# Optimization experiments

Hardware: AMD Instinct MI355X
Metric: run time of the kernel (lower is better)

Reference implementation:

```python
import jax, jax.numpy as jnp
import numpy as np

B, S, D = 1, 2048, 1024
H, HD = 16, 64          # attention heads, head dim
DFF = 4096              # ffn hidden
IH, ID = 4, 64          # indexer heads / dim ('baseline' strategy)
TOP_K = 64
ROPE_BASE = 10000.0
LN_EPS = 1e-5


def setup_inputs() -> dict:
    key = jax.random.key(0)
    ks = jax.random.split(key, 12)
    g = lambda k, shape: (jax.random.normal(k, shape, dtype=jnp.float32) * 0.02)
    return {
        "x": jax.random.normal(ks[0], (B, S, D), dtype=jnp.float32),
        "w_qkv": g(ks[1], (D, 3 * D)),
        "w_o": g(ks[2], (D, D)),
        "ffn_w1": g(ks[3], (D, DFF)),
        "ffn_b1": jnp.zeros((DFF,), jnp.float32),
        "ffn_w2": g(ks[4], (DFF, D)),
        "ffn_b2": jnp.zeros((D,), jnp.float32),
        "ln1_g": jnp.ones((D,), jnp.float32),
        "ln1_b": jnp.zeros((D,), jnp.float32),
        "ln2_g": jnp.ones((D,), jnp.float32),
        "ln2_b": jnp.zeros((D,), jnp.float32),
        "idx_wq": g(ks[5], (D, IH * ID)),
        "idx_wk": g(ks[6], (D, ID)),
        "idx_ww": g(ks[7], (D, IH)),
    }


def _layernorm(x, g, b):
    m = jnp.mean(x, axis=-1, keepdims=True)
    v = jnp.var(x, axis=-1, keepdims=True)
    return (x - m) * jax.lax.rsqrt(v + LN_EPS) * g + b


def _rope(x):  # x: [B,S,H,HD], torchtune interleaved-pair convention
    half = HD // 2
    theta = 1.0 / (ROPE_BASE ** (jnp.arange(0, HD, 2, dtype=jnp.float32) / HD))  # [half]
    ang = jnp.arange(S, dtype=jnp.float32)[:, None] * theta                      # [S,half]
    cos = jnp.cos(ang)[None, :, None, :]
    sin = jnp.sin(ang)[None, :, None, :]
    xp = x.reshape(*x.shape[:-1], half, 2)
    x0, x1 = xp[..., 0], xp[..., 1]
    out = jnp.stack([x0 * cos - x1 * sin, x1 * cos + x0 * sin], axis=-1)
    return out.reshape(x.shape)


def reference(x, w_qkv, w_o, ffn_w1, ffn_b1, ffn_w2, ffn_b2,
              ln1_g, ln1_b, ln2_g, ln2_b, idx_wq, idx_wk, idx_ww):
    norm_x = _layernorm(x, ln1_g, ln1_b)

    qkv = norm_x @ w_qkv                              # [B,S,3D]
    q, k, v = jnp.split(qkv, 3, axis=-1)
    q = _rope(q.reshape(B, S, H, HD))
    k = _rope(k.reshape(B, S, H, HD))
    v = v.reshape(B, S, H, HD)

    # Lightning-style indexer: I[t,s] = sum_h w[t,h] * relu(q_i[t,h] . k_i[s])
    qi = (norm_x @ idx_wq).reshape(B, S, IH, ID)      # [B,S,IH,ID]
    ki = norm_x @ idx_wk                              # [B,S,ID]
    wi = norm_x @ idx_ww                              # [B,S,IH]
    qk = jnp.einsum("bthd,bsd->bths", qi, ki)         # [B,S,IH,S]
    index_scores = jnp.einsum("bth,bths->bts", wi, jax.nn.relu(qk))  # [B,S,S]

    # causal top-k token selection -> boolean mask
    causal = jnp.tril(jnp.ones((S, S), dtype=bool))
    masked_scores = jnp.where(causal, index_scores, -jnp.inf)
    _, topk_idx = jax.lax.top_k(masked_scores, TOP_K)  # [B,S,K]
    b_ix = jnp.arange(B)[:, None, None]
    q_ix = jnp.arange(S)[None, :, None]
    mask = jnp.zeros((B, S, S), dtype=bool).at[b_ix, q_ix, topk_idx].set(True)
    mask = mask & causal                               # [B,S,S]

    # masked SDPA
    logits = jnp.einsum("bqhd,bkhd->bhqk", q, k) / np.sqrt(HD)
    logits = jnp.where(mask[:, None, :, :], logits, -jnp.inf)
    attn = jax.nn.softmax(logits, axis=-1)
    attn_out = jnp.einsum("bhqk,bkhd->bqhd", attn, v).reshape(B, S, D)
    x = x + attn_out @ w_o

    h = _layernorm(x, ln2_g, ln2_b)
    ffn = jax.nn.gelu(h @ ffn_w1 + ffn_b1, approximate=False) @ ffn_w2 + ffn_b2
    return x + ffn
```

## Files before the change

kernel.cpp:

```cpp
#include <hip/hip_runtime.h>
#include <math.h>

#define S_LEN 2048
#define D_MODEL 1024
#define NHEAD 16
#define HDIM 64
#define DFF 4096
#define IH 4
#define IDM 64
#define TOPK 64
#define NIDX 336

typedef float f32x4 __attribute__((ext_vector_type(4)));
typedef short bf16x8 __attribute__((ext_vector_type(8)));

__device__ __forceinline__ unsigned short f2bf(float f) {
    unsigned u = __builtin_bit_cast(unsigned, f);
    u += 0x7fff + ((u >> 16) & 1);
    return (unsigned short)(u >> 16);
}
__device__ __forceinline__ float bf2f(unsigned short us) {
    return __builtin_bit_cast(float, (unsigned)us << 16);
}

__device__ __forceinline__ float gelu_exact(float v) {
    return 0.5f * v * (1.f + erff(v * 0.70710678118654752f));
}

__device__ __forceinline__ void gl_lds16(const void* g, void* l) {
    __builtin_amdgcn_global_load_lds(
        (const __attribute__((address_space(1))) void*)g,
        (__attribute__((address_space(3))) void*)l, 16, 0, 0);
}

__global__ __launch_bounds__(256) void ln_kernel(const float* __restrict__ x,
    const float* __restrict__ g, const float* __restrict__ b,
    float* __restrict__ outf, unsigned short* __restrict__ outb)
{
    int row = blockIdx.x, tid = threadIdx.x;
    const float4 v = *(const float4*)(x + (size_t)row * D_MODEL + tid * 4);
    float s = v.x + v.y + v.z + v.w;
    float ss = v.x * v.x + v.y * v.y + v.z * v.z + v.w * v.w;
    int lane = tid & 63, wv = tid >> 6;
    for (int o = 32; o; o >>= 1) { s += __shfl_xor(s, o); ss += __shfl_xor(ss, o); }
    __shared__ float rs[4], rss[4];
    if (lane == 0) { rs[wv] = s; rss[wv] = ss; }
    __syncthreads();
    float S = rs[0] + rs[1] + rs[2] + rs[3];
    float SS = rss[0] + rss[1] + rss[2] + rss[3];
    float mean = S * (1.f / D_MODEL);
    float var = SS * (1.f / D_MODEL) - mean * mean;
    float r = rsqrtf(var + 1e-5f);
    float4 gv = *(const float4*)(g + tid * 4);
    float4 bv = *(const float4*)(b + tid * 4);
    float4 o4;
    o4.x = (v.x - mean) * r * gv.x + bv.x;
    o4.y = (v.y - mean) * r * gv.y + bv.y;
    o4.z = (v.z - mean) * r * gv.z + bv.z;
    o4.w = (v.w - mean) * r * gv.w + bv.w;
    if (outf) *(float4*)(outf + (size_t)row * D_MODEL + tid * 4) = o4;
    if (outb) {
        ushort4 u4 = { f2bf(o4.x), f2bf(o4.y), f2bf(o4.z), f2bf(o4.w) };
        *(ushort4*)(outb + (size_t)row * D_MODEL + tid * 4) = u4;
    }
}

__global__ __launch_bounds__(256) void wo_ln2_kernel(const float* __restrict__ Pwo,
    const float* __restrict__ x, const float* __restrict__ g, const float* __restrict__ b,
    float* __restrict__ outf, unsigned short* __restrict__ outb)
{
    int row = blockIdx.x, tid = threadIdx.x;
    size_t MN = (size_t)S_LEN * D_MODEL;
    size_t off = (size_t)row * D_MODEL + tid * 4;
    float4 p0 = *(const float4*)(Pwo + off);
    float4 p1 = *(const float4*)(Pwo + MN + off);
    float4 xr = *(const float4*)(x + off);
    float4 v;
    v.x = p0.x + p1.x + xr.x;
    v.y = p0.y + p1.y + xr.y;
    v.z = p0.z + p1.z + xr.z;
    v.w = p0.w + p1.w + xr.w;
    *(float4*)(outf + off) = v;
    float s = v.x + v.y + v.z + v.w;
    float ss = v.x * v.x + v.y * v.y + v.z * v.z + v.w * v.w;
    int lane = tid & 63, wv = tid >> 6;
    for (int o = 32; o; o >>= 1) { s += __shfl_xor(s, o); ss += __shfl_xor(ss, o); }
    __shared__ float rs[4], rss[4];
    if (lane == 0) { rs[wv] = s; rss[wv] = ss; }
    __syncthreads();
    float S = rs[0] + rs[1] + rs[2] + rs[3];
    float SS = rss[0] + rss[1] + rss[2] + rss[3];
    float mean = S * (1.f / D_MODEL);
    float var = SS * (1.f / D_MODEL) - mean * mean;
    float r = rsqrtf(var + 1e-5f);
    float4 gv = *(const float4*)(g + tid * 4);
    float4 bv = *(const float4*)(b + tid * 4);
    ushort4 u4 = { f2bf((v.x - mean) * r * gv.x + bv.x),
                   f2bf((v.y - mean) * r * gv.y + bv.y),
                   f2bf((v.z - mean) * r * gv.z + bv.z),
                   f2bf((v.w - mean) * r * gv.w + bv.w) };
    *(ushort4*)(outb + off) = u4;
}

__device__ __forceinline__ void wtrans_body(const float* __restrict__ in,
    unsigned short* __restrict__ out, int K, int N, int bx, int by, int tid)
{
    __shared__ float t[32][33];
    int k0 = by * 32, n0 = bx * 32;
    int r = tid >> 5, c = tid & 31;
#pragma unroll
    for (int p = 0; p < 4; ++p)
        t[r + p * 8][c] = in[(size_t)(k0 + r + p * 8) * N + n0 + c];
    __syncthreads();
#pragma unroll
    for (int p = 0; p < 4; ++p)
        out[(size_t)(n0 + r + p * 8) * K + k0 + c] = f2bf(t[c][r + p * 8]);
}

#define PREP_ROPE   256
#define PREP_WQKV   3072
#define PREP_WO     1024
#define PREP_W1     4096
#define PREP_W2     4096
#define PREP_WPACK  1344
#define PREP_TOTAL  (PREP_ROPE + PREP_WQKV + PREP_WO + PREP_W1 + PREP_W2 + PREP_WPACK)
__global__ __launch_bounds__(256) void prep_kernel(
    const float* __restrict__ w_qkv, const float* __restrict__ w_o,
    const float* __restrict__ w1, const float* __restrict__ w2,
    const float* __restrict__ wq, const float* __restrict__ wk, const float* __restrict__ ww,
    unsigned short* __restrict__ wqkv_t, unsigned short* __restrict__ wo_t,
    unsigned short* __restrict__ w1_t, unsigned short* __restrict__ w2_t,
    float* __restrict__ Wc, float* __restrict__ ct, float* __restrict__ st)
{
    int b = blockIdx.x, tid = threadIdx.x;
    if (b < PREP_ROPE) {
        int g = b * 256 + tid;
        int t = g >> 5, i = g & 31;
        float theta = powf(10000.f, -(float)i / 32.f);
        float ang = (float)t * theta;
        ct[g] = cosf(ang);
        st[g] = sinf(ang);
        return;
    }
    b -= PREP_ROPE;
    if (b < PREP_WQKV) { wtrans_body(w_qkv, wqkv_t, 1024, 3072, b % 96, b / 96, tid); return; }
    b -= PREP_WQKV;
    if (b < PREP_WO)   { wtrans_body(w_o, wo_t, 1024, 1024, b % 32, b / 32, tid); return; }
    b -= PREP_WO;
    if (b < PREP_W1)   { wtrans_body(w1, w1_t, 1024, 4096, b % 128, b / 128, tid); return; }
    b -= PREP_W1;
    if (b < PREP_W2)   { wtrans_body(w2, w2_t, 4096, 1024, b % 32, b / 32, tid); return; }
    b -= PREP_W2;
    {
        int idx = b * 256 + tid;
        if (idx >= D_MODEL * NIDX) return;
        int r = idx / NIDX, c = idx % NIDX;
        float v = 0.f;
        if (c < 256) v = wq[r * 256 + c];
        else if (c < 320) v = wk[r * 64 + (c - 256)];
        else if (c < 324) v = ww[r * 4 + (c - 320)];
        Wc[idx] = v;
    }
}

__global__ __launch_bounds__(256) void gemm_bf16_n64(
    const unsigned short* __restrict__ A, const unsigned short* __restrict__ Bt,
    float* __restrict__ C, unsigned short* __restrict__ Cb,
    const float* __restrict__ bias, const float* __restrict__ R,
    int M, int N, int K, int act,
    float* __restrict__ P, int kchunk)
{
    __shared__ __attribute__((aligned(16))) unsigned short As[3][128 * 32];
    __shared__ __attribute__((aligned(16))) unsigned short Bs[3][64 * 32];
    int tid = threadIdx.x;
    int bm = blockIdx.y * 128, bn = blockIdx.x * 64;
    int wid = tid >> 6, lane = tid & 63;
    int wm = wid * 32;
    const unsigned short* Ab = A + (size_t)bm * K;
    const unsigned short* Bb = Bt + (size_t)bn * K;
    f32x4 acc[2][4];
#pragma unroll
    for (int i = 0; i < 2; ++i)
#pragma unroll
        for (int j = 0; j < 4; ++j)
            acc[i][j] = (f32x4){0.f, 0.f, 0.f, 0.f};

    int kbeg = blockIdx.z * kchunk;
    int NT = kchunk >> 5;
    int fr = lane & 15, fk = (lane >> 4) * 8;
    int e0 = tid * 8;
    int r0 = e0 >> 5, c0 = e0 & 31;

    auto STAGE = [&](int kt, int buf) {
        int k0 = kbeg + kt * 32;
        gl_lds16(Ab + (size_t)r0 * K + k0 + c0, &As[buf][e0]);
        gl_lds16(Ab + (size_t)(r0 + 64) * K + k0 + c0, &As[buf][e0 + 2048]);
        gl_lds16(Bb + (size_t)r0 * K + k0 + c0, &Bs[buf][e0]);
    };
    auto COMPUTE = [&](int buf) {
        bf16x8 af[2], bfv[4];
#pragma unroll
        for (int mi = 0; mi < 2; ++mi)
            af[mi] = *(const bf16x8*)&As[buf][(wm + mi * 16 + fr) * 32 + fk];
#pragma unroll
        for (int ni = 0; ni < 4; ++ni)
            bfv[ni] = *(const bf16x8*)&Bs[buf][(ni * 16 + fr) * 32 + fk];
#pragma unroll
        for (int mi = 0; mi < 2; ++mi)
#pragma unroll
            for (int ni = 0; ni < 4; ++ni)
                acc[mi][ni] = __builtin_amdgcn_mfma_f32_16x16x32_bf16(
                    af[mi], bfv[ni], acc[mi][ni], 0, 0, 0);
    };

    STAGE(0, 0);
    STAGE(1, 1);
    asm volatile("s_waitcnt vmcnt(3)" ::: "memory");
    __builtin_amdgcn_s_barrier();

    for (int kt = 0; kt < NT - 2; ++kt) {
        STAGE(kt + 2, (kt + 2) % 3);
        COMPUTE(kt % 3);
        asm volatile("s_waitcnt vmcnt(3)" ::: "memory");
        __builtin_amdgcn_s_barrier();
    }
    COMPUTE((NT - 2) % 3);
    asm volatile("s_waitcnt vmcnt(0)" ::: "memory");
    __builtin_amdgcn_s_barrier();
    COMPUTE((NT - 1) % 3);

    int cl = lane & 15, rh = (lane >> 4) * 4;
    if (P) {
        float* Pz = P + (size_t)blockIdx.z * M * N;
#pragma unroll
        for (int mi = 0; mi < 2; ++mi)
#pragma unroll
            for (int ni = 0; ni < 4; ++ni) {
                int col = bn + ni * 16 + cl;
#pragma unroll
                for (int r = 0; r < 4; ++r) {
                    int row = bm + wm + mi * 16 + rh + r;
                    Pz[(size_t)row * N + col] = acc[mi][ni][r];
                }
            }
        return;
    }
#pragma unroll
    for (int mi = 0; mi < 2; ++mi) {
#pragma unroll
        for (int ni = 0; ni < 4; ++ni) {
            int col = bn + ni * 16 + cl;
            float bv = bias ? bias[col] : 0.f;
#pragma unroll
            for (int r = 0; r < 4; ++r) {
                int row = bm + wm + mi * 16 + rh + r;
                float v = acc[mi][ni][r] + bv;
                if (act) v = gelu_exact(v);
                size_t off = (size_t)row * N + col;
                if (R) v += R[off];
                if (C) C[off] = v;
                if (Cb) Cb[off] = f2bf(v);
            }
        }
    }
}

#define DUAL_QKV 768
__global__ __launch_bounds__(256) void dual_qkv_idx_kernel(
    const unsigned short* __restrict__ A, const unsigned short* __restrict__ Bt,
    unsigned short* __restrict__ Cb,
    const float* __restrict__ Af, const float* __restrict__ Bf, float* __restrict__ P)
{
    __shared__ __attribute__((aligned(16))) unsigned char ldsbuf[36864];
    int b = blockIdx.x, tid = threadIdx.x;
    if (b < DUAL_QKV) {
        const int K = D_MODEL, N = 3 * D_MODEL;
        unsigned short (*As)[128 * 32] = (unsigned short (*)[128 * 32])ldsbuf;
        unsigned short (*Bs)[64 * 32] = (unsigned short (*)[64 * 32])(ldsbuf + 3 * 128 * 32 * 2);
        int bx = b % 48, by = b / 48;
        int bm = by * 128, bn = bx * 64;
        int wid = tid >> 6, lane = tid & 63;
        int wm = wid * 32;
        const unsigned short* Ab = A + (size_t)bm * K;
        const unsigned short* Bb = Bt + (size_t)bn * K;
        f32x4 acc[2][4];
#pragma unroll
        for (int i = 0; i < 2; ++i)
#pragma unroll
            for (int j = 0; j < 4; ++j)
                acc[i][j] = (f32x4){0.f, 0.f, 0.f, 0.f};
        int NT = K >> 5;
        int fr = lane & 15, fk = (lane >> 4) * 8;
        int e0 = tid * 8;
        int r0 = e0 >> 5, c0 = e0 & 31;
        auto STAGE = [&](int kt, int buf) {
            int k0 = kt * 32;
            gl_lds16(Ab + (size_t)r0 * K + k0 + c0, &As[buf][e0]);
            gl_lds16(Ab + (size_t)(r0 + 64) * K + k0 + c0, &As[buf][e0 + 2048]);
            gl_lds16(Bb + (size_t)r0 * K + k0 + c0, &Bs[buf][e0]);
        };
        auto COMPUTE = [&](int buf) {
            bf16x8 af[2], bfv[4];
#pragma unroll
            for (int mi = 0; mi < 2; ++mi)
                af[mi] = *(const bf16x8*)&As[buf][(wm + mi * 16 + fr) * 32 + fk];
#pragma unroll
            for (int ni = 0; ni < 4; ++ni)
                bfv[ni] = *(const bf16x8*)&Bs[buf][(ni * 16 + fr) * 32 + fk];
#pragma unroll
            for (int mi = 0; mi < 2; ++mi)
#pragma unroll
                for (int ni = 0; ni < 4; ++ni)
                    acc[mi][ni] = __builtin_amdgcn_mfma_f32_16x16x32_bf16(
                        af[mi], bfv[ni], acc[mi][ni], 0, 0, 0);
        };
        STAGE(0, 0);
        STAGE(1, 1);
        asm volatile("s_waitcnt vmcnt(3)" ::: "memory");
        __builtin_amdgcn_s_barrier();
        for (int kt = 0; kt < NT - 2; ++kt) {
            STAGE(kt + 2, (kt + 2) % 3);
            COMPUTE(kt % 3);
            asm volatile("s_waitcnt vmcnt(3)" ::: "memory");
            __builtin_amdgcn_s_barrier();
        }
        COMPUTE((NT - 2) % 3);
        asm volatile("s_waitcnt vmcnt(0)" ::: "memory");
        __builtin_amdgcn_s_barrier();
        COMPUTE((NT - 1) % 3);
        int cl = lane & 15, rh = (lane >> 4) * 4;
#pragma unroll
        for (int mi = 0; mi < 2; ++mi)
#pragma unroll
            for (int ni = 0; ni < 4; ++ni) {
                int col = bn + ni * 16 + cl;
#pragma unroll
                for (int r = 0; r < 4; ++r) {
                    int row = bm + wm + mi * 16 + rh + r;
                    Cb[(size_t)row * N + col] = f2bf(acc[mi][ni][r]);
                }
            }
    } else {
        const int M = S_LEN, N = NIDX, K = D_MODEL, kchunk = D_MODEL / 4;
        float (*As)[68] = (float (*)[68])ldsbuf;
        float (*Bs)[68] = (float (*)[68])(ldsbuf + 16 * 68 * 4);
        int b2 = b - DUAL_QKV;
        int bn = b2 % 6, bm = (b2 / 6) % 32, bz = b2 / 192;
        int tx = tid & 15, ty = tid >> 4;
        int arow = tid >> 2;
        int acol = (tid & 3) << 2;
        int brow = tid >> 4;
        int bcol = (tid & 15) << 2;
        const float* Abase = Af + (size_t)(bm * 64 + arow) * K + acol;
        float c[4][4] = {};
        int kbeg = bz * kchunk;
        int kend = kbeg + kchunk;
        for (int k0 = kbeg; k0 < kend; k0 += 16) {
            float4 av = *(const float4*)(Abase + k0);
            As[acol + 0][arow] = av.x;
            As[acol + 1][arow] = av.y;
            As[acol + 2][arow] = av.z;
            As[acol + 3][arow] = av.w;
            int gcol = bn * 64 + bcol;
            const float* Bb = Bf + (size_t)(k0 + brow) * N;
            float4 bv;
            if (gcol + 3 < N) {
                bv = *(const float4*)(Bb + gcol);
            } else {
                bv.x = (gcol + 0 < N) ? Bb[gcol + 0] : 0.f;
                bv.y = (gcol + 1 < N) ? Bb[gcol + 1] : 0.f;
                bv.z = (gcol + 2 < N) ? Bb[gcol + 2] : 0.f;
                bv.w = (gcol + 3 < N) ? Bb[gcol + 3] : 0.f;
            }
            *(float4*)&Bs[brow][bcol] = bv;
            __syncthreads();
#pragma unroll
            for (int kk = 0; kk < 16; ++kk) {
                float4 a4 = *(const float4*)&As[kk][ty * 4];
                float4 b4 = *(const float4*)&Bs[kk][tx * 4];
                float av4[4] = { a4.x, a4.y, a4.z, a4.w };
                float bv4[4] = { b4.x, b4.y, b4.z, b4.w };
#pragma unroll
                for (int i = 0; i < 4; ++i)
#pragma unroll
                    for (int j = 0; j < 4; ++j)
                        c[i][j] += av4[i] * bv4[j];
            }
            __syncthreads();
        }
        float* Out = P + (size_t)bz * M * N;
#pragma unroll
        for (int i = 0; i < 4; ++i) {
            int row = bm * 64 + ty * 4 + i;
#pragma unroll
            for (int j = 0; j < 4; ++j) {
                int col = bn * 64 + tx * 4 + j;
                if (col < N)
                    Out[(size_t)row * N + col] = c[i][j];
            }
        }
    }
}

__global__ __launch_bounds__(256) void kreduce_kernel(const float* __restrict__ P,
    int nslice, float* __restrict__ C, const float* __restrict__ bias,
    const float* __restrict__ R, int M, int N)
{
    size_t total4 = (size_t)M * N / 4;
    size_t stride = (size_t)gridDim.x * 256;
    for (size_t i4 = blockIdx.x * 256 + threadIdx.x; i4 < total4; i4 += stride) {
        size_t off = i4 * 4;
        float4 v = *(const float4*)(P + off);
        for (int z = 1; z < nslice; ++z) {
            float4 p = *(const float4*)(P + (size_t)z * M * N + off);
            v.x += p.x; v.y += p.y; v.z += p.z; v.w += p.w;
        }
        if (bias) {
            float4 b4 = *(const float4*)(bias + (off % N));
            v.x += b4.x; v.y += b4.y; v.z += b4.z; v.w += b4.w;
        }
        if (R) {
            float4 r4 = *(const float4*)(R + off);
            v.x += r4.x; v.y += r4.y; v.z += r4.z; v.w += r4.w;
        }
        *(float4*)(C + off) = v;
    }
}

__global__ __launch_bounds__(512) void rope_pack_kernel(
    const unsigned short* __restrict__ qkvb,
    const float* __restrict__ ct, const float* __restrict__ st,
    unsigned short* __restrict__ Qb, unsigned short* __restrict__ Kb,
    unsigned short* __restrict__ Vb)
{
    int t = blockIdx.x, tid = threadIdx.x;
    int h = tid >> 5, i = tid & 31;
    float c = ct[t * 32 + i], s = st[t * 32 + i];
    const unsigned short* base = qkvb + (size_t)t * (3 * D_MODEL);
    ushort2 q2 = *(const ushort2*)(base + h * HDIM + 2 * i);
    float q0 = bf2f(q2.x), q1 = bf2f(q2.y);
    ushort2 qo = { f2bf(q0 * c - q1 * s), f2bf(q1 * c + q0 * s) };
    *(ushort2*)(Qb + (size_t)t * D_MODEL + h * HDIM + 2 * i) = qo;
    ushort2 k2 = *(const ushort2*)(base + D_MODEL + h * HDIM + 2 * i);
    float k0 = bf2f(k2.x), k1 = bf2f(k2.y);
    ushort2 ko = { f2bf(k0 * c - k1 * s), f2bf(k1 * c + k0 * s) };
    *(ushort2*)(Kb + ((size_t)h * S_LEN + t) * HDIM + 2 * i) = ko;
    ushort2 v2 = *(const ushort2*)(base + 2 * D_MODEL + 2 * tid);
    int vh = tid >> 5, vd = (2 * tid) & 63;
    *(ushort2*)(Vb + ((size_t)vh * S_LEN + t) * HDIM + vd) = v2;
}

__global__ __launch_bounds__(256) void scores_kernel(const float* __restrict__ QIW,
    float* __restrict__ scores)
{
    int t0 = blockIdx.y * 64, s0 = blockIdx.x * 64;
    if (s0 > t0 + 63) return;
    __shared__ float qit[64][68];
    __shared__ float kit[64][68];
    __shared__ float wis[64][4];
    int tid = threadIdx.x;
    int tx = tid & 15, ty = tid >> 4;
    int lr = tid & 63;
    int cseg = tid >> 6;
    if (tid < 64) {
        float4 w4 = *(const float4*)(QIW + (size_t)(t0 + tid) * NIDX + 320);
        wis[tid][0] = w4.x; wis[tid][1] = w4.y; wis[tid][2] = w4.z; wis[tid][3] = w4.w;
    }
    float acc[4][4] = {};
#pragma unroll
    for (int h = 0; h < 4; ++h) {
        __syncthreads();
        const float* qrow = QIW + (size_t)(t0 + lr) * NIDX + h * 64 + cseg * 16;
        const float* krow = QIW + (size_t)(s0 + lr) * NIDX + 256 + cseg * 16;
#pragma unroll
        for (int q4 = 0; q4 < 4; ++q4) {
            int d = cseg * 16 + q4 * 4;
            float4 v = *(const float4*)(qrow + q4 * 4);
            qit[d + 0][lr] = v.x; qit[d + 1][lr] = v.y;
            qit[d + 2][lr] = v.z; qit[d + 3][lr] = v.w;
            if (h == 0) {
                float4 u = *(const float4*)(krow + q4 * 4);
                kit[d + 0][lr] = u.x; kit[d + 1][lr] = u.y;
                kit[d + 2][lr] = u.z; kit[d + 3][lr] = u.w;
            }
        }
        __syncthreads();
        float dot[4][4] = {};
#pragma unroll 8
        for (int d = 0; d < 64; ++d) {
            float4 a4 = *(const float4*)&qit[d][ty * 4];
            float4 b4 = *(const float4*)&kit[d][tx * 4];
            float av[4] = { a4.x, a4.y, a4.z, a4.w };
            float bv[4] = { b4.x, b4.y, b4.z, b4.w };
#pragma unroll
            for (int i = 0; i < 4; ++i)
#pragma unroll
                for (int j = 0; j < 4; ++j)
                    dot[i][j] += av[i] * bv[j];
        }
#pragma unroll
        for (int i = 0; i < 4; ++i) {
            float w = wis[ty * 4 + i][h];
#pragma unroll
            for (int j = 0; j < 4; ++j)
                acc[i][j] += w * fmaxf(dot[i][j], 0.f);
        }
    }
#pragma unroll
    for (int i = 0; i < 4; ++i) {
        float4 o4 = { acc[i][0], acc[i][1], acc[i][2], acc[i][3] };
        *(float4*)&scores[(size_t)(t0 + ty * 4 + i) * S_LEN + s0 + tx * 4] = o4;
    }
}

__global__ __launch_bounds__(256) void topk_kernel(const float* __restrict__ scores,
    int* __restrict__ topidx, int* __restrict__ topcnt)
{
    int t = blockIdx.x, tid = threadIdx.x;
    int n = t + 1;
    if (n <= TOPK) {
        if (tid < n) topidx[t * TOPK + tid] = tid;
        if (tid == 0) topcnt[t] = n;
        return;
    }
    __shared__ unsigned sc[S_LEN];
    __shared__ unsigned hist[256];
    __shared__ int selbin_s;
    __shared__ int cnt_out;
    __shared__ unsigned wsum[4];
    for (int j = tid; j < n; j += 256) {
        unsigned u = __builtin_bit_cast(unsigned, scores[(size_t)t * S_LEN + j]);
        sc[j] = (u & 0x80000000u) ? ~u : (u | 0x80000000u);
    }
    if (tid == 0) cnt_out = 0;
    int lane = tid & 63, wv = tid >> 6;
    unsigned prefix = 0;
    int kk = TOPK;
#pragma unroll
    for (int round = 0; round < 4; ++round) {
        int shift_pref = 32 - 8 * round;
        int shift_bin = 24 - 8 * round;
        hist[tid] = 0;
        __syncthreads();
        for (int j = tid; j < n; j += 256) {
            unsigned v = sc[j];
            if ((((unsigned long long)(v ^ prefix)) >> shift_pref) == 0)
                atomicAdd(&hist[(v >> shift_bin) & 0xff], 1u);
        }
        __syncthreads();
        if (wv == 0) {
            unsigned h0 = hist[4 * lane], h1 = hist[4 * lane + 1];
            unsigned h2 = hist[4 * lane + 2], h3 = hist[4 * lane + 3];
            unsigned s3 = h3, s2 = h2 + s3, s1 = h1 + s2, s0 = h0 + s1;
            unsigned acc = s0;
            for (int off = 1; off < 64; off <<= 1) {
                unsigned o = __shfl_down(acc, off);
                if (lane + off < 64) acc += o;
            }
            unsigned above = acc - s0;
            hist[4 * lane]     = s0 + above;
            hist[4 * lane + 1] = s1 + above;
            hist[4 * lane + 2] = s2 + above;
            hist[4 * lane + 3] = s3 + above;
        }
        __syncthreads();
        {
            unsigned sufb = hist[tid];
            unsigned sufn = (tid < 255) ? hist[tid + 1] : 0u;
            if (sufb >= (unsigned)kk && sufn < (unsigned)kk)
                selbin_s = tid;
        }
        __syncthreads();
        int b = selbin_s;
        unsigned above = (b < 255) ? hist[b + 1] : 0u;
        kk -= (int)above;
        prefix |= ((unsigned)b) << shift_bin;
        __syncthreads();
    }
    unsigned T = prefix;
    int chunk = (n + 255) >> 8;
    int jb = tid * chunk;
    int je = jb + chunk; if (je > n) je = n;
    int ties = 0;
    for (int j = jb; j < je; ++j) {
        unsigned v = sc[j];
        if (v > T) { int o = atomicAdd(&cnt_out, 1); topidx[t * TOPK + o] = j; }
        else if (v == T) ++ties;
    }
    unsigned inc = (unsigned)ties;
    for (int off = 1; off < 64; off <<= 1) {
        unsigned o = __shfl_up(inc, off);
        if (lane >= off) inc += o;
    }
    if (lane == 63) wsum[wv] = inc;
    __syncthreads();
    unsigned woff = 0;
    for (int w = 0; w < wv; ++w) woff += wsum[w];
    int rank = (int)(woff + inc) - ties;
    for (int j = jb; j < je && rank < kk; ++j) {
        if (sc[j] == T) {
            int o = atomicAdd(&cnt_out, 1);
            topidx[t * TOPK + o] = j;
            ++rank;
        }
    }
    if (tid == 0) topcnt[t] = TOPK;
}

__global__ __launch_bounds__(256) void attn_kernel(
    const unsigned short* __restrict__ Qb, const unsigned short* __restrict__ Kb,
    const unsigned short* __restrict__ Vb,
    const int* __restrict__ topidx, const int* __restrict__ topcnt,
    unsigned short* __restrict__ out)
{
    int t = blockIdx.x, tid = threadIdx.x;
    __shared__ int sel[TOPK];
    if (tid < TOPK) sel[tid] = topidx[t * TOPK + tid];
    __syncthreads();
    int cnt = topcnt[t];
    int lane = tid & 63, wv = tid >> 6;
    int h = blockIdx.y * 4 + wv;
    int klo = lane >> 3, oct = lane & 7;
    int rows[8];
    bool valid[8];
#pragma unroll
    for (int kg = 0; kg < 8; ++kg) {
        int k = kg * 8 + klo;
        valid[kg] = (k < cnt);
        rows[kg] = sel[valid[kg] ? k : 0];
    }
    bf16x8 q8 = *(const bf16x8*)(Qb + (size_t)t * D_MODEL + h * HDIM + oct * 8);
    float qf[8];
#pragma unroll
    for (int e = 0; e < 8; ++e) qf[e] = bf2f((unsigned short)q8[e]);

    const unsigned short* kbase = Kb + (size_t)h * S_LEN * HDIM + oct * 8;
    float p[8];
#pragma unroll
    for (int kg = 0; kg < 8; ++kg) {
        bf16x8 k8 = *(const bf16x8*)(kbase + (size_t)rows[kg] * HDIM);
        float d = 0.f;
#pragma unroll
        for (int e = 0; e < 8; ++e)
            d += bf2f((unsigned short)k8[e]) * qf[e];
        d += __shfl_xor(d, 1);
        d += __shfl_xor(d, 2);
        d += __shfl_xor(d, 4);
        p[kg] = valid[kg] ? d * 0.125f : -INFINITY;
    }
    float m = p[0];
#pragma unroll
    for (int kg = 1; kg < 8; ++kg) m = fmaxf(m, p[kg]);
    m = fmaxf(m, __shfl_xor(m, 8));
    m = fmaxf(m, __shfl_xor(m, 16));
    m = fmaxf(m, __shfl_xor(m, 32));
    float sum = 0.f;
#pragma unroll
    for (int kg = 0; kg < 8; ++kg) { p[kg] = __expf(p[kg] - m); sum += p[kg]; }
    sum += __shfl_xor(sum, 8);
    sum += __shfl_xor(sum, 16);
    sum += __shfl_xor(sum, 32);
    float rs = 1.f / sum;
    const unsigned short* vbase = Vb + (size_t)h * S_LEN * HDIM + oct * 8;
    float facc[8] = {};
#pragma unroll
    for (int kg = 0; kg < 8; ++kg) {
        bf16x8 v8 = *(const bf16x8*)(vbase + (size_t)rows[kg] * HDIM);
        float pw = p[kg] * rs;
#pragma unroll
        for (int e = 0; e < 8; ++e)
            facc[e] += pw * bf2f((unsigned short)v8[e]);
    }
#pragma unroll
    for (int e = 0; e < 8; ++e) {
        facc[e] += __shfl_xor(facc[e], 8);
        facc[e] += __shfl_xor(facc[e], 16);
        facc[e] += __shfl_xor(facc[e], 32);
    }
    if (klo == 0) {
        ushort4 o0 = { f2bf(facc[0]), f2bf(facc[1]), f2bf(facc[2]), f2bf(facc[3]) };
        ushort4 o1 = { f2bf(facc[4]), f2bf(facc[5]), f2bf(facc[6]), f2bf(facc[7]) };
        *(ushort4*)(out + (size_t)t * D_MODEL + h * HDIM + oct * 8) = o0;
        *(ushort4*)(out + (size_t)t * D_MODEL + h * HDIM + oct * 8 + 4) = o1;
    }
}

extern "C" void kernel_launch(void* const* d_in, const int* in_sizes, int n_in,
                              void* d_out, int out_size, void* d_ws, size_t ws_size,
                              hipStream_t stream)
{
    const float* x      = (const float*)d_in[0];
    const float* w_qkv  = (const float*)d_in[1];
    const float* w_o    = (const float*)d_in[2];
    const float* ffn_w1 = (const float*)d_in[3];
    const float* ffn_b1 = (const float*)d_in[4];
    const float* ffn_w2 = (const float*)d_in[5];
    const float* ffn_b2 = (const float*)d_in[6];
    const float* ln1_g  = (const float*)d_in[7];
    const float* ln1_b  = (const float*)d_in[8];
    const float* ln2_g  = (const float*)d_in[9];
    const float* ln2_b  = (const float*)d_in[10];
    const float* idx_wq = (const float*)d_in[11];
    const float* idx_wk = (const float*)d_in[12];
    const float* idx_ww = (const float*)d_in[13];
    float* outp = (float*)d_out;

    const size_t MB = 1ull << 20;
    char* ws = (char*)d_ws;
    float*          normx    = (float*)(ws + 0);
    unsigned short* attno_bf = (unsigned short*)(ws + 0);
    float*          Pf2      = (float*)(ws + 0);
    unsigned short* normx_bf = (unsigned short*)(ws + 8 * MB);
    unsigned short* h2_bf    = normx_bf;
    unsigned short* qkv_bf   = (unsigned short*)(ws + 12 * MB);
    int*            topidx   = (int*)(ws + 12 * MB);
    int*            topcnt   = (int*)(ws + 12 * MB + 512 * 1024);
    unsigned short* wqkv_t   = (unsigned short*)(ws + 24 * MB);
    unsigned short* wo_t     = (unsigned short*)(ws + 30 * MB);
    unsigned short* w1_t     = (unsigned short*)(ws + 32 * MB);
    unsigned short* w2_t     = (unsigned short*)(ws + 40 * MB);
    float*          P_idx    = (float*)(ws + 48 * MB);
    unsigned short* Qb       = (unsigned short*)(ws + 48 * MB);
    unsigned short* Kb       = (unsigned short*)(ws + 52 * MB);
    unsigned short* Vb       = (unsigned short*)(ws + 56 * MB);
    float*          ctab     = (float*)(ws + 60 * MB);
    float*          stab     = (float*)(ws + 60 * MB + 256 * 1024);
    float*          scoresb  = (float*)(ws + 60 * MB);
    float*          Pwo      = (float*)(ws + 60 * MB);
    unsigned short* ffn1_bf  = (unsigned short*)(ws + 60 * MB);
    float*          QIW      = (float*)(ws + 76 * MB);
    float*          Wc       = (float*)(ws + 79 * MB);

    dim3 blk256(256);
    auto g64n = [](int N, int M) { return dim3(N / 64, M / 128); };

    ln_kernel<<<S_LEN, blk256, 0, stream>>>(x, ln1_g, ln1_b, normx, normx_bf);
    prep_kernel<<<PREP_TOTAL, blk256, 0, stream>>>(w_qkv, w_o, ffn_w1, ffn_w2,
        idx_wq, idx_wk, idx_ww, wqkv_t, wo_t, w1_t, w2_t, Wc, ctab, stab);
    dual_qkv_idx_kernel<<<DUAL_QKV + 768, blk256, 0, stream>>>(normx_bf, wqkv_t, qkv_bf,
        normx, Wc, P_idx);
    kreduce_kernel<<<1024, blk256, 0, stream>>>(P_idx, 4, QIW, nullptr, nullptr, S_LEN, NIDX);
    rope_pack_kernel<<<S_LEN, dim3(512), 0, stream>>>(qkv_bf, ctab, stab, Qb, Kb, Vb);
    scores_kernel<<<dim3(32, 32), blk256, 0, stream>>>(QIW, scoresb);
    topk_kernel<<<S_LEN, blk256, 0, stream>>>(scoresb, topidx, topcnt);
    attn_kernel<<<dim3(S_LEN, 4), blk256, 0, stream>>>(Qb, Kb, Vb, topidx, topcnt, attno_bf);
    gemm_bf16_n64<<<dim3(D_MODEL / 64, S_LEN / 128, 2), blk256, 0, stream>>>(attno_bf, wo_t,
        nullptr, nullptr, nullptr, nullptr, S_LEN, D_MODEL, D_MODEL, 0, Pwo, D_MODEL / 2);
    wo_ln2_kernel<<<S_LEN, blk256, 0, stream>>>(Pwo, x, ln2_g, ln2_b, outp, h2_bf);
    gemm_bf16_n64<<<g64n(DFF, S_LEN), blk256, 0, stream>>>(h2_bf, w1_t,
        nullptr, ffn1_bf, ffn_b1, nullptr, S_LEN, DFF, D_MODEL, 1, nullptr, D_MODEL);
    gemm_bf16_n64<<<dim3(D_MODEL / 64, S_LEN / 128, 4), blk256, 0, stream>>>(ffn1_bf, w2_t,
        nullptr, nullptr, nullptr, nullptr, S_LEN, D_MODEL, DFF, 0, Pf2, DFF / 4);
    kreduce_kernel<<<1024, blk256, 0, stream>>>(Pf2, 4, outp, ffn_b2, outp, S_LEN, D_MODEL);
}
```

Before: 265.4 us.

## Fuse RoPE and Q/K/V packing into QKV GEMM epilogue, split indexer GEMM

The QKV bf16 MFMA GEMM now applies RoPE in its epilogue, using a lane shuffle to fetch the paired element, and writes Q, K and V straight into their packed per-head layouts. This removes the separate rope_pack kernel and the round trip of the intermediate qkv buffer through global memory. The fp32 indexer projection, which was co-scheduled inside the same launch, becomes its own gemm64 launch, so the two workloads no longer share one grid and there is one more kernel launch. Scattered per-head stores in the epilogue may be less coalesced, and RoPE is applied before the bf16 rounding rather than after it.

```diff
diff --git a/kernel.cpp b/kernel.cpp
--- a/kernel.cpp
+++ b/kernel.cpp
@@ -265,140 +265,105 @@
     }
 }
 
-#define DUAL_QKV 768
-__global__ __launch_bounds__(256) void dual_qkv_idx_kernel(
+__global__ __launch_bounds__(256) void gemm_qkv_rope(
     const unsigned short* __restrict__ A, const unsigned short* __restrict__ Bt,
-    unsigned short* __restrict__ Cb,
-    const float* __restrict__ Af, const float* __restrict__ Bf, float* __restrict__ P)
-{
-    __shared__ __attribute__((aligned(16))) unsigned char ldsbuf[36864];
-    int b = blockIdx.x, tid = threadIdx.x;
-    if (b < DUAL_QKV) {
-        const int K = D_MODEL, N = 3 * D_MODEL;
-        unsigned short (*As)[128 * 32] = (unsigned short (*)[128 * 32])ldsbuf;
-        unsigned short (*Bs)[64 * 32] = (unsigned short (*)[64 * 32])(ldsbuf + 3 * 128 * 32 * 2);
-        int bx = b % 48, by = b / 48;
-        int bm = by * 128, bn = bx * 64;
-        int wid = tid >> 6, lane = tid & 63;
-        int wm = wid * 32;
-        const unsigned short* Ab = A + (size_t)bm * K;
-        const unsigned short* Bb = Bt + (size_t)bn * K;
-        f32x4 acc[2][4];
-#pragma unroll
-        for (int i = 0; i < 2; ++i)
-#pragma unroll
-            for (int j = 0; j < 4; ++j)
-                acc[i][j] = (f32x4){0.f, 0.f, 0.f, 0.f};
-        int NT = K >> 5;
-        int fr = lane & 15, fk = (lane >> 4) * 8;
-        int e0 = tid * 8;
-        int r0 = e0 >> 5, c0 = e0 & 31;
-        auto STAGE = [&](int kt, int buf) {
-            int k0 = kt * 32;
-            gl_lds16(Ab + (size_t)r0 * K + k0 + c0, &As[buf][e0]);
-            gl_lds16(Ab + (size_t)(r0 + 64) * K + k0 + c0, &As[buf][e0 + 2048]);
-            gl_lds16(Bb + (size_t)r0 * K + k0 + c0, &Bs[buf][e0]);
-        };
-        auto COMPUTE = [&](int buf) {
-            bf16x8 af[2], bfv[4];
-#pragma unroll
-            for (int mi = 0; mi < 2; ++mi)
-                af[mi] = *(const bf16x8*)&As[buf][(wm + mi * 16 + fr) * 32 + fk];
+    const float* __restrict__ ct, const float* __restrict__ st,
+    unsigned short* __restrict__ Qb, unsigned short* __restrict__ Kb,
+    unsigned short* __restrict__ Vb)
+{
+    const int K = D_MODEL, NT = D_MODEL / 32;
+    __shared__ __attribute__((aligned(16))) unsigned short As[3][128 * 32];
+    __shared__ __attribute__((aligned(16))) unsigned short Bs[3][64 * 32];
+    int tid = threadIdx.x;
+    int bm = blockIdx.y * 128, bn = blockIdx.x * 64;
+    int wid = tid >> 6, lane = tid & 63;
+    int wm = wid * 32;
+    const unsigned short* Ab = A + (size_t)bm * K;
+    const unsigned short* Bb = Bt + (size_t)bn * K;
+    f32x4 acc[2][4];
+#pragma unroll
+    for (int i = 0; i < 2; ++i)
+#pragma unroll
+        for (int j = 0; j < 4; ++j)
+            acc[i][j] = (f32x4){0.f, 0.f, 0.f, 0.f};
+
+    int fr = lane & 15, fk = (lane >> 4) * 8;
+    int e0 = tid * 8;
+    int r0 = e0 >> 5, c0 = e0 & 31;
+
+    auto STAGE = [&](int kt, int buf) {
+        int k0 = kt * 32;
+        gl_lds16(Ab + (size_t)r0 * K + k0 + c0, &As[buf][e0]);
+        gl_lds16(Ab + (size_t)(r0 + 64) * K + k0 + c0, &As[buf][e0 + 2048]);
+        gl_lds16(Bb + (size_t)r0 * K + k0 + c0, &Bs[buf][e0]);
+    };
+    auto COMPUTE = [&](int buf) {
+        bf16x8 af[2], bfv[4];
+#pragma unroll
+        for (int mi = 0; mi < 2; ++mi)
+            af[mi] = *(const bf16x8*)&As[buf][(wm + mi * 16 + fr) * 32 + fk];
+#pragma unroll
+        for (int ni = 0; ni < 4; ++ni)
+            bfv[ni] = *(const bf16x8*)&Bs[buf][(ni * 16 + fr) * 32 + fk];
+#pragma unroll
+        for (int mi = 0; mi < 2; ++mi)
 #pragma unroll
             for (int ni = 0; ni < 4; ++ni)
-                bfv[ni] = *(const bf16x8*)&Bs[buf][(ni * 16 + fr) * 32 + fk];
-#pragma unroll
-            for (int mi = 0; mi < 2; ++mi)
-#pragma unroll
-                for (int ni = 0; ni < 4; ++ni)
-                    acc[mi][ni] = __builtin_amdgcn_mfma_f32_16x16x32_bf16(
-                        af[mi], bfv[ni], acc[mi][ni], 0, 0, 0);
-        };
-        STAGE(0, 0);
-        STAGE(1, 1);
+                acc[mi][ni] = __builtin_amdgcn_mfma_f32_16x16x32_bf16(
+                    af[mi], bfv[ni], acc[mi][ni], 0, 0, 0);
+    };
+
+    STAGE(0, 0);
+    STAGE(1, 1);
+    asm volatile("s_waitcnt vmcnt(3)" ::: "memory");
+    __builtin_amdgcn_s_barrier();
+    for (int kt = 0; kt < NT - 2; ++kt) {
+        STAGE(kt + 2, (kt + 2) % 3);
+        COMPUTE(kt % 3);
         asm volatile("s_waitcnt vmcnt(3)" ::: "memory");
         __builtin_amdgcn_s_barrier();
-        for (int kt = 0; kt < NT - 2; ++kt) {
-            STAGE(kt + 2, (kt + 2) % 3);
-            COMPUTE(kt % 3);
-            asm volatile("s_waitcnt vmcnt(3)" ::: "memory");
-            __builtin_amdgcn_s_barrier();
-        }
-        COMPUTE((NT - 2) % 3);
-        asm volatile("s_waitcnt vmcnt(0)" ::: "memory");
-        __builtin_amdgcn_s_barrier();
-        COMPUTE((NT - 1) % 3);
-        int cl = lane & 15, rh = (lane >> 4) * 4;
+    }
+    COMPUTE((NT - 2) % 3);
+    asm volatile("s_waitcnt vmcnt(0)" ::: "memory");
+    __builtin_amdgcn_s_barrier();
+    COMPUTE((NT - 1) % 3);
+
+    int cl = lane & 15, rh = (lane >> 4) * 4;
+    int region = bn >> 10;
+    int hh = (bn & 1023) >> 6;
+    if (region == 2) {
 #pragma unroll
         for (int mi = 0; mi < 2; ++mi)
 #pragma unroll
             for (int ni = 0; ni < 4; ++ni) {
-                int col = bn + ni * 16 + cl;
+                int d = ni * 16 + cl;
 #pragma unroll
                 for (int r = 0; r < 4; ++r) {
                     int row = bm + wm + mi * 16 + rh + r;
-                    Cb[(size_t)row * N + col] = f2bf(acc[mi][ni][r]);
+                    Vb[((size_t)hh * S_LEN + row) * HDIM + d] = f2bf(acc[mi][ni][r]);
                 }
             }
     } else {
-        const int M = S_LEN, N = NIDX, K = D_MODEL, kchunk = D_MODEL / 4;
-        float (*As)[68] = (float (*)[68])ldsbuf;
-        float (*Bs)[68] = (float (*)[68])(ldsbuf + 16 * 68 * 4);
-        int b2 = b - DUAL_QKV;
-        int bn = b2 % 6, bm = (b2 / 6) % 32, bz = b2 / 192;
-        int tx = tid & 15, ty = tid >> 4;
-        int arow = tid >> 2;
-        int acol = (tid & 3) << 2;
-        int brow = tid >> 4;
-        int bcol = (tid & 15) << 2;
-        const float* Abase = Af + (size_t)(bm * 64 + arow) * K + acol;
-        float c[4][4] = {};
-        int kbeg = bz * kchunk;
-        int kend = kbeg + kchunk;
-        for (int k0 = kbeg; k0 < kend; k0 += 16) {
-            float4 av = *(const float4*)(Abase + k0);
-            As[acol + 0][arow] = av.x;
-            As[acol + 1][arow] = av.y;
-            As[acol + 2][arow] = av.z;
-            As[acol + 3][arow] = av.w;
-            int gcol = bn * 64 + bcol;
-            const float* Bb = Bf + (size_t)(k0 + brow) * N;
-            float4 bv;
-            if (gcol + 3 < N) {
-                bv = *(const float4*)(Bb + gcol);
-            } else {
-                bv.x = (gcol + 0 < N) ? Bb[gcol + 0] : 0.f;
-                bv.y = (gcol + 1 < N) ? Bb[gcol + 1] : 0.f;
-                bv.z = (gcol + 2 < N) ? Bb[gcol + 2] : 0.f;
-                bv.w = (gcol + 3 < N) ? Bb[gcol + 3] : 0.f;
+#pragma unroll
+        for (int mi = 0; mi < 2; ++mi)
+#pragma unroll
+            for (int ni = 0; ni < 4; ++ni) {
+                int d = ni * 16 + cl;
+                int i = d >> 1;
+                bool odd = d & 1;
+#pragma unroll
+                for (int r = 0; r < 4; ++r) {
+                    int row = bm + wm + mi * 16 + rh + r;
+                    float v = acc[mi][ni][r];
+                    float p = __shfl_xor(v, 1);
+                    float c = ct[row * 32 + i], s = st[row * 32 + i];
+                    float o = odd ? (v * c + p * s) : (v * c - p * s);
+                    if (region == 0)
+                        Qb[(size_t)row * D_MODEL + bn + d] = f2bf(o);
+                    else
+                        Kb[((size_t)hh * S_LEN + row) * HDIM + d] = f2bf(o);
+                }
             }
-            *(float4*)&Bs[brow][bcol] = bv;
-            __syncthreads();
-#pragma unroll
-            for (int kk = 0; kk < 16; ++kk) {
-                float4 a4 = *(const float4*)&As[kk][ty * 4];
-                float4 b4 = *(const float4*)&Bs[kk][tx * 4];
-                float av4[4] = { a4.x, a4.y, a4.z, a4.w };
-                float bv4[4] = { b4.x, b4.y, b4.z, b4.w };
-#pragma unroll
-                for (int i = 0; i < 4; ++i)
-#pragma unroll
-                    for (int j = 0; j < 4; ++j)
-                        c[i][j] += av4[i] * bv4[j];
-            }
-            __syncthreads();
-        }
-        float* Out = P + (size_t)bz * M * N;
-#pragma unroll
-        for (int i = 0; i < 4; ++i) {
-            int row = bm * 64 + ty * 4 + i;
-#pragma unroll
-            for (int j = 0; j < 4; ++j) {
-                int col = bn * 64 + tx * 4 + j;
-                if (col < N)
-                    Out[(size_t)row * N + col] = c[i][j];
-            }
-        }
     }
 }
 
@@ -427,27 +392,68 @@
     }
 }
 
-__global__ __launch_bounds__(512) void rope_pack_kernel(
-    const unsigned short* __restrict__ qkvb,
-    const float* __restrict__ ct, const float* __restrict__ st,
-    unsigned short* __restrict__ Qb, unsigned short* __restrict__ Kb,
-    unsigned short* __restrict__ Vb)
-{
-    int t = blockIdx.x, tid = threadIdx.x;
-    int h = tid >> 5, i = tid & 31;
-    float c = ct[t * 32 + i], s = st[t * 32 + i];
-    const unsigned short* base = qkvb + (size_t)t * (3 * D_MODEL);
-    ushort2 q2 = *(const ushort2*)(base + h * HDIM + 2 * i);
-    float q0 = bf2f(q2.x), q1 = bf2f(q2.y);
-    ushort2 qo = { f2bf(q0 * c - q1 * s), f2bf(q1 * c + q0 * s) };
-    *(ushort2*)(Qb + (size_t)t * D_MODEL + h * HDIM + 2 * i) = qo;
-    ushort2 k2 = *(const ushort2*)(base + D_MODEL + h * HDIM + 2 * i);
-    float k0 = bf2f(k2.x), k1 = bf2f(k2.y);
-    ushort2 ko = { f2bf(k0 * c - k1 * s), f2bf(k1 * c + k0 * s) };
-    *(ushort2*)(Kb + ((size_t)h * S_LEN + t) * HDIM + 2 * i) = ko;
-    ushort2 v2 = *(const ushort2*)(base + 2 * D_MODEL + 2 * tid);
-    int vh = tid >> 5, vd = (2 * tid) & 63;
-    *(ushort2*)(Vb + ((size_t)vh * S_LEN + t) * HDIM + vd) = v2;
+__global__ __launch_bounds__(256) void gemm64(const float* __restrict__ A,
+    const float* __restrict__ B, float* __restrict__ C,
+    int M, int N, int K,
+    float* __restrict__ P, int kchunk)
+{
+    __shared__ float As[16][68];
+    __shared__ float Bs[16][68];
+    int tid = threadIdx.x;
+    int bm = blockIdx.y, bn = blockIdx.x;
+    int tx = tid & 15, ty = tid >> 4;
+    int arow = tid >> 2;
+    int acol = (tid & 3) << 2;
+    int brow = tid >> 4;
+    int bcol = (tid & 15) << 2;
+    const float* Abase = A + (size_t)(bm * 64 + arow) * K + acol;
+    float c[4][4] = {};
+    int kbeg = blockIdx.z * kchunk;
+    int kend = kbeg + kchunk;
+    for (int k0 = kbeg; k0 < kend; k0 += 16) {
+        float4 av = *(const float4*)(Abase + k0);
+        As[acol + 0][arow] = av.x;
+        As[acol + 1][arow] = av.y;
+        As[acol + 2][arow] = av.z;
+        As[acol + 3][arow] = av.w;
+        int gcol = bn * 64 + bcol;
+        const float* Bb = B + (size_t)(k0 + brow) * N;
+        float4 bv;
+        if (gcol + 3 < N) {
+            bv = *(const float4*)(Bb + gcol);
+        } else {
+            bv.x = (gcol + 0 < N) ? Bb[gcol + 0] : 0.f;
+            bv.y = (gcol + 1 < N) ? Bb[gcol + 1] : 0.f;
+            bv.z = (gcol + 2 < N) ? Bb[gcol + 2] : 0.f;
+            bv.w = (gcol + 3 < N) ? Bb[gcol + 3] : 0.f;
+        }
+        *(float4*)&Bs[brow][bcol] = bv;
+        __syncthreads();
+#pragma unroll
+        for (int kk = 0; kk < 16; ++kk) {
+            float4 a4 = *(const float4*)&As[kk][ty * 4];
+            float4 b4 = *(const float4*)&Bs[kk][tx * 4];
+            float av4[4] = { a4.x, a4.y, a4.z, a4.w };
+            float bv4[4] = { b4.x, b4.y, b4.z, b4.w };
+#pragma unroll
+            for (int i = 0; i < 4; ++i)
+#pragma unroll
+                for (int j = 0; j < 4; ++j)
+                    c[i][j] += av4[i] * bv4[j];
+        }
+        __syncthreads();
+    }
+    float* Out = P ? (P + (size_t)blockIdx.z * M * N) : C;
+#pragma unroll
+    for (int i = 0; i < 4; ++i) {
+        int row = bm * 64 + ty * 4 + i;
+#pragma unroll
+        for (int j = 0; j < 4; ++j) {
+            int col = bn * 64 + tx * 4 + j;
+            if (col < N)
+                Out[(size_t)row * N + col] = c[i][j];
+        }
+    }
 }
 
 __global__ __launch_bounds__(256) void scores_kernel(const float* __restrict__ QIW,
@@ -712,19 +718,18 @@
     float*          Pf2      = (float*)(ws + 0);
     unsigned short* normx_bf = (unsigned short*)(ws + 8 * MB);
     unsigned short* h2_bf    = normx_bf;
-    unsigned short* qkv_bf   = (unsigned short*)(ws + 12 * MB);
     int*            topidx   = (int*)(ws + 12 * MB);
     int*            topcnt   = (int*)(ws + 12 * MB + 512 * 1024);
     unsigned short* wqkv_t   = (unsigned short*)(ws + 24 * MB);
     unsigned short* wo_t     = (unsigned short*)(ws + 30 * MB);
     unsigned short* w1_t     = (unsigned short*)(ws + 32 * MB);
     unsigned short* w2_t     = (unsigned short*)(ws + 40 * MB);
-    float*          P_idx    = (float*)(ws + 48 * MB);
     unsigned short* Qb       = (unsigned short*)(ws + 48 * MB);
     unsigned short* Kb       = (unsigned short*)(ws + 52 * MB);
     unsigned short* Vb       = (unsigned short*)(ws + 56 * MB);
     float*          ctab     = (float*)(ws + 60 * MB);
     float*          stab     = (float*)(ws + 60 * MB + 256 * 1024);
+    float*          P_idx    = (float*)(ws + 61 * MB);
     float*          scoresb  = (float*)(ws + 60 * MB);
     float*          Pwo      = (float*)(ws + 60 * MB);
     unsigned short* ffn1_bf  = (unsigned short*)(ws + 60 * MB);
@@ -737,10 +742,11 @@
     ln_kernel<<<S_LEN, blk256, 0, stream>>>(x, ln1_g, ln1_b, normx, normx_bf);
     prep_kernel<<<PREP_TOTAL, blk256, 0, stream>>>(w_qkv, w_o, ffn_w1, ffn_w2,
         idx_wq, idx_wk, idx_ww, wqkv_t, wo_t, w1_t, w2_t, Wc, ctab, stab);
-    dual_qkv_idx_kernel<<<DUAL_QKV + 768, blk256, 0, stream>>>(normx_bf, wqkv_t, qkv_bf,
-        normx, Wc, P_idx);
+    gemm_qkv_rope<<<g64n(3 * D_MODEL, S_LEN), blk256, 0, stream>>>(normx_bf, wqkv_t,
+        ctab, stab, Qb, Kb, Vb);
+    gemm64<<<dim3((NIDX + 63) / 64, S_LEN / 64, 4), blk256, 0, stream>>>(normx, Wc,
+        nullptr, S_LEN, NIDX, D_MODEL, P_idx, D_MODEL / 4);
     kreduce_kernel<<<1024, blk256, 0, stream>>>(P_idx, 4, QIW, nullptr, nullptr, S_LEN, NIDX);
-    rope_pack_kernel<<<S_LEN, dim3(512), 0, stream>>>(qkv_bf, ctab, stab, Qb, Kb, Vb);
     scores_kernel<<<dim3(32, 32), blk256, 0, stream>>>(QIW, scoresb);
     topk_kernel<<<S_LEN, blk256, 0, stream>>>(scoresb, topidx, topcnt);
     attn_kernel<<<dim3(S_LEN, 4), blk256, 0, stream>>>(Qb, Kb, Vb, topidx, topcnt, attno_bf);
```

After: 260.0 us. 2.0% less time.
